# Kernel optimization log

Measured on AMD Instinct MI355X. Metric: run time of the kernel, lower is better.

Reference implementation:

```python
import jax, jax.numpy as jnp
import numpy as np

B, D = 32768, 512
L, K = 4, 1024


def setup_inputs() -> dict:
    key = jax.random.key(0)
    kz, kc = jax.random.split(key)
    z = jax.random.normal(kz, (B, D), dtype=jnp.float32)
    # nn.Parameter(torch.randn(L, K, D) * 0.1)
    codebooks = jax.random.normal(kc, (L, K, D), dtype=jnp.float32) * 0.1
    return {"z": z, "codebooks": codebooks}


def reference(z, codebooks):
    # z: [B, D], codebooks: [L, K, D]
    num_levels = codebooks.shape[0]
    residual = z
    level_vecs = []
    rq_loss = jnp.float32(0.0)
    for l in range(num_levels):  # small fixed L, structurally distinct levels
        cb = codebooks[l]  # [K, D]
        # squared euclidean distance via ||r||^2 - 2 r.c + ||c||^2 (same math as
        # sum((r[:,None]-c[None])**2, -1), avoids the [B,K,D] broadcast intermediate)
        r2 = jnp.sum(residual * residual, axis=-1, keepdims=True)      # [B, 1]
        c2 = jnp.sum(cb * cb, axis=-1)                                  # [K]
        dist = r2 - 2.0 * (residual @ cb.T) + c2                        # [B, K]
        idx = jnp.argmin(dist, axis=-1)                                 # [B]
        chosen = cb[idx]                                                # [B, D]
        level_vecs.append(chosen)
        residual = residual - chosen
        # F.mse_loss(residual.detach(), zeros) -> mean of squared residual, no grad
        rq_loss = rq_loss + jnp.mean(jax.lax.stop_gradient(residual) ** 2)
    all_level_vectors = jnp.stack(level_vecs, axis=0)  # [L, B, D]
    quantized = all_level_vectors.sum(axis=0)          # [B, D]
    return (quantized, all_level_vectors, rq_loss)
```

## Files before the change

kernel.cpp:

```cpp
#include <hip/hip_runtime.h>

#define BROWS 32768
#define DIM   512
#define NK    1024
#define NL    4

typedef _Float16 f16;
typedef _Float16 f16x8 __attribute__((ext_vector_type(8)));
typedef float f32x4 __attribute__((ext_vector_type(4)));

#define LSC 2.44140625e-4f

union H4 { f16 h[4]; ushort4 u; };

__device__ __forceinline__ void split2(float x, f16& h, f16& l) {
  h = (f16)x;
  l = (f16)((x - (float)h) * 4096.0f);
}

__device__ __forceinline__ void gload16(const void* g, const void* l) {
  __builtin_amdgcn_global_load_lds(
      (const __attribute__((address_space(1))) void*)g,
      (__attribute__((address_space(3))) void*)l, 16, 0, 0);
}

__global__ __launch_bounds__(64) void k_pre(const float* __restrict__ cb,
                                            float* __restrict__ c2all,
                                            float* __restrict__ loss_slot,
                                            f16* __restrict__ cbI) {
  const int code = blockIdx.x;
  const int lane = threadIdx.x;
  const float4* c4 = (const float4*)(cb + (size_t)code * DIM);
  f16* rowL = cbI + (size_t)code * 1024;
  float s = 0.f;
#pragma unroll
  for (int j = 0; j < 2; ++j) {
    const int e = lane + j * 64;
    const float4 v = c4[e];
    s += v.x * v.x + v.y * v.y + v.z * v.z + v.w * v.w;
    H4 hh, ll;
#pragma unroll
    for (int c = 0; c < 4; ++c) split2((&v.x)[c], hh.h[c], ll.h[c]);
    *(ushort4*)(rowL + e * 4) = hh.u;
    *(ushort4*)(rowL + 512 + e * 4) = ll.u;
  }
#pragma unroll
  for (int m = 1; m < 64; m <<= 1) s += __shfl_xor(s, m, 64);
  if (lane == 0) c2all[code] = s;
  if (code == 0 && lane == 0) *loss_slot = 0.f;
}

__global__ __launch_bounds__(256) void k_splitz(const float* __restrict__ Z,
                                                float* __restrict__ r2,
                                                f16* __restrict__ RL) {
  const int t = threadIdx.x;
  const int row = blockIdx.x * 8 + (t >> 5);
  const int lane = t & 31;
  const float4* z4 = (const float4*)(Z + (size_t)row * DIM);
  f16* rowL = RL + (size_t)row * 1024;
  float s = 0.f;
#pragma unroll
  for (int j = 0; j < 4; ++j) {
    const int e = lane + j * 32;
    const float4 v = z4[e];
    s += v.x * v.x + v.y * v.y + v.z * v.z + v.w * v.w;
    H4 hh, ll;
#pragma unroll
    for (int c = 0; c < 4; ++c) split2((&v.x)[c], hh.h[c], ll.h[c]);
    *(ushort4*)(rowL + e * 4) = hh.u;
    *(ushort4*)(rowL + 512 + e * 4) = ll.u;
  }
#pragma unroll
  for (int m = 1; m < 32; m <<= 1) s += __shfl_xor(s, m, 64);
  if (lane == 0) r2[row] = s;
}

__global__ __launch_bounds__(256, 2) void k_gemm(
    const f16* __restrict__ A,
    const f16* __restrict__ Bc,
    const float* __restrict__ r2v, const float* __restrict__ c2v,
    float* __restrict__ pmin, int* __restrict__ pidx) {
  __shared__ __align__(16) char smem[2][32768];

  const int t = threadIdx.x;
  const int lane = t & 63, wid = t >> 6;
  const int wr = wid >> 1, wc = wid & 1;
  const int lin = blockIdx.y * 8 + blockIdx.x;
  const int xcd = lin & 7, kk8 = lin >> 3;
  const int mb = xcd * 32 + (kk8 >> 3);
  const int nb = kk8 & 7;
  const int rowBase = mb * 128, colBase = nb * 128;
  const int l15 = lane & 15, kg = lane >> 4;

  const char* gA[4]; const char* gB[4];
  int ldsA[4], ldsB[4];
#pragma unroll
  for (int i = 0; i < 4; ++i) {
    const int g = i * 256 + wid * 64 + lane;
    const int r = g >> 3;
    const int u = (g & 7) ^ (r & 7);
    const size_t off = (size_t)r * 2048 + (size_t)(u >> 2) * 1024 + (u & 3) * 16;
    gA[i] = (const char*)A + (size_t)rowBase * 2048 + off;
    gB[i] = (const char*)Bc + (size_t)colBase * 2048 + off;
    ldsA[i] = i * 4096 + wid * 1024;
    ldsB[i] = 16384 + i * 4096 + wid * 1024;
  }

  const f32x4 zero = {0.f, 0.f, 0.f, 0.f};
  f32x4 accH[4][4], accL[4][4];
#pragma unroll
  for (int i = 0; i < 4; ++i)
#pragma unroll
    for (int j = 0; j < 4; ++j) { accH[i][j] = zero; accL[i][j] = zero; }

  auto stage = [&](int buf, int kt) {
    char* s = &smem[buf][0];
#pragma unroll
    for (int i = 0; i < 4; ++i) {
      gload16(gA[i] + kt * 64, s + ldsA[i]);
      gload16(gB[i] + kt * 64, s + ldsB[i]);
    }
  };

  auto compute = [&](int buf) {
    const char* sA = &smem[buf][0];
    const char* sB = sA + 16384;
    f16x8 bhv[4], blv[4];
#pragma unroll
    for (int ni = 0; ni < 4; ++ni) {
      const int c = wc * 64 + ni * 16 + l15;
      const int x = c & 7;
      bhv[ni] = *(const f16x8*)(sB + c * 128 + ((kg ^ x) << 4));
      blv[ni] = *(const f16x8*)(sB + c * 128 + (((4 + kg) ^ x) << 4));
    }
#pragma unroll
    for (int mi = 0; mi < 4; ++mi) {
      const int r = wr * 64 + mi * 16 + l15;
      const int x = r & 7;
      const f16x8 ahv = *(const f16x8*)(sA + r * 128 + ((kg ^ x) << 4));
      const f16x8 alw = *(const f16x8*)(sA + r * 128 + (((4 + kg) ^ x) << 4));
#pragma unroll
      for (int ni = 0; ni < 4; ++ni) {
        accH[mi][ni] = __builtin_amdgcn_mfma_f32_16x16x32_f16(ahv, bhv[ni], accH[mi][ni], 0, 0, 0);
        accL[mi][ni] = __builtin_amdgcn_mfma_f32_16x16x32_f16(ahv, blv[ni], accL[mi][ni], 0, 0, 0);
        accL[mi][ni] = __builtin_amdgcn_mfma_f32_16x16x32_f16(alw, bhv[ni], accL[mi][ni], 0, 0, 0);
      }
    }
  };

  stage(0, 0);
  for (int kt = 0; kt < 16; ++kt) {
    __syncthreads();
    if (kt < 15) stage((kt + 1) & 1, kt + 1);
    compute(kt & 1);
  }

  float* redm = (float*)&smem[0][0];
  int* redi = (int*)(&smem[0][0] + 1024);
  float c2c[4];
#pragma unroll
  for (int ni = 0; ni < 4; ++ni) c2c[ni] = c2v[colBase + wc * 64 + ni * 16 + l15];
#pragma unroll
  for (int mi = 0; mi < 4; ++mi) {
#pragma unroll
    for (int j = 0; j < 4; ++j) {
      const int rloc = wr * 64 + mi * 16 + kg * 4 + j;
      const float r2r = r2v[rowBase + rloc];
      float bm = 3.4e38f; int bi = 0x7fffffff;
#pragma unroll
      for (int ni = 0; ni < 4; ++ni) {
        const int col = colBase + wc * 64 + ni * 16 + l15;
        const float dot = accH[mi][ni][j] + accL[mi][ni][j] * LSC;
        const float dist = (r2r - 2.0f * dot) + c2c[ni];
        if (dist < bm || (dist == bm && col < bi)) { bm = dist; bi = col; }
      }
#pragma unroll
      for (int m = 1; m < 16; m <<= 1) {
        const float om = __shfl_xor(bm, m, 64);
        const int oi = __shfl_xor(bi, m, 64);
        if (om < bm || (om == bm && oi < bi)) { bm = om; bi = oi; }
      }
      if (l15 == 0) { redm[rloc * 2 + wc] = bm; redi[rloc * 2 + wc] = bi; }
    }
  }
  __syncthreads();
  if (t < 128) {
    float bm = redm[t * 2]; int bi = redi[t * 2];
    const float m1 = redm[t * 2 + 1]; const int i1 = redi[t * 2 + 1];
    if (m1 < bm || (m1 == bm && i1 < bi)) { bm = m1; bi = i1; }
    pmin[(size_t)nb * BROWS + rowBase + t] = bm;
    pidx[(size_t)nb * BROWS + rowBase + t] = bi;
  }
}

__global__ __launch_bounds__(256) void k_update(f16* RL,
                                                const float* __restrict__ CB,
                                                const float* __restrict__ pminv,
                                                const int* __restrict__ pidxv,
                                                float* __restrict__ chosen_out,
                                                float* __restrict__ r2out,
                                                float* __restrict__ loss,
                                                const float* __restrict__ Z,
                                                float* Q,
                                                int last) {
  __shared__ float ls[8];
  const int t = threadIdx.x;
  const int rrow = t >> 5, lane = t & 31;
  const int row = blockIdx.x * 8 + rrow;

  float bm = 3.4e38f;
  int bi = 0x7fffffff;
#pragma unroll
  for (int nbk = 0; nbk < 8; ++nbk) {
    const float m = pminv[(size_t)nbk * BROWS + row];
    const int i = pidxv[(size_t)nbk * BROWS + row];
    if (m < bm || (m == bm && i < bi)) { bm = m; bi = i; }
  }

  f16* rowL = RL + (size_t)row * 1024;
  ushort4 hu[4], lu[4];
#pragma unroll
  for (int j = 0; j < 4; ++j) {
    const int e = lane + j * 32;
    hu[j] = *(const ushort4*)(rowL + e * 4);
    lu[j] = *(const ushort4*)(rowL + 512 + e * 4);
  }

  const float4* c4 = (const float4*)(CB + (size_t)bi * DIM);
  float4* ch4 = (float4*)(chosen_out + (size_t)row * DIM);
  float s = 0.f;
#pragma unroll
  for (int j = 0; j < 4; ++j) {
    const int e = lane + j * 32;
    const float4 c = c4[e];
    H4 hh, llv;
    hh.u = hu[j]; llv.u = lu[j];
    float4 rn;
    rn.x = ((float)hh.h[0] + (float)llv.h[0] * LSC) - c.x;
    rn.y = ((float)hh.h[1] + (float)llv.h[1] * LSC) - c.y;
    rn.z = ((float)hh.h[2] + (float)llv.h[2] * LSC) - c.z;
    rn.w = ((float)hh.h[3] + (float)llv.h[3] * LSC) - c.w;
    ch4[e] = c;
    if (!last) {
      H4 nh, nl;
#pragma unroll
      for (int cc = 0; cc < 4; ++cc) split2((&rn.x)[cc], nh.h[cc], nl.h[cc]);
      *(ushort4*)(rowL + e * 4) = nh.u;
      *(ushort4*)(rowL + 512 + e * 4) = nl.u;
    } else {
      const float4 zv = ((const float4*)(Z + (size_t)row * DIM))[e];
      float4 qq;
      qq.x = zv.x - rn.x; qq.y = zv.y - rn.y; qq.z = zv.z - rn.z; qq.w = zv.w - rn.w;
      ((float4*)(Q + (size_t)row * DIM))[e] = qq;
    }
    s += rn.x * rn.x + rn.y * rn.y + rn.z * rn.z + rn.w * rn.w;
  }
#pragma unroll
  for (int m = 1; m < 32; m <<= 1) s += __shfl_xor(s, m, 64);
  if (lane == 0) {
    if (!last) r2out[row] = s;
    ls[rrow] = s;
  }
  __syncthreads();
  if (t == 0) {
    float tot = 0.f;
#pragma unroll
    for (int i = 0; i < 8; ++i) tot += ls[i];
    atomicAdd(loss, tot * (1.0f / 16777216.0f));
  }
}

extern "C" void kernel_launch(void* const* d_in, const int* in_sizes, int n_in,
                              void* d_out, int out_size, void* d_ws, size_t ws_size,
                              hipStream_t stream) {
  const float* z  = (const float*)d_in[0];
  const float* cb = (const float*)d_in[1];

  float* q    = (float*)d_out;
  float* alv  = (float*)d_out + (size_t)BROWS * DIM;
  float* loss = (float*)d_out + (size_t)BROWS * DIM * (NL + 1);

  float* c2all = (float*)d_ws;
  float* r2ws  = c2all + NL * NK;
  float* pmin  = r2ws + BROWS;
  int*   pidx  = (int*)(pmin + 8 * BROWS);
  f16*   cbI   = (f16*)(pidx + 8 * BROWS);

  f16* RL = (f16*)q;

  k_pre<<<NL * NK, 64, 0, stream>>>(cb, c2all, loss, cbI);
  k_splitz<<<BROWS / 8, 256, 0, stream>>>(z, r2ws, RL);

  for (int l = 0; l < NL; ++l) {
    k_gemm<<<dim3(8, 256), 256, 0, stream>>>(RL, cbI + (size_t)l * NK * 1024,
                                             r2ws, c2all + l * NK, pmin, pidx);
    const int last = (l == NL - 1);
    k_update<<<BROWS / 8, 256, 0, stream>>>(RL, cb + (size_t)l * NK * DIM,
                                            pmin, pidx,
                                            alv + (size_t)l * BROWS * DIM,
                                            r2ws, loss, z, q, last);
  }
}
```

Measured before the change: 1.087 ms.

## Shrink GEMM tile to 64x128 with 1x4 wave layout for higher occupancy

Changes the distance GEMM block tile from 128x128 to 64x128 rows by columns. All four waves now split the columns, 32 each, and the grid doubles to 8x512 blocks. LDS per block drops from 64KB to 48KB and the accumulator count halves, and launch bounds are raised to 3 blocks per CU so more waves can hide latency. In exchange, each codebook tile is reused across fewer rows, so more B traffic goes through global and LDS per FLOP. The final reduction now combines four column partials, and a barrier is added before the shared memory is reused.

```diff
diff --git a/kernel.cpp b/kernel.cpp
--- a/kernel.cpp
+++ b/kernel.cpp
@@ -75,76 +75,85 @@
   if (lane == 0) r2[row] = s;
 }
 
-__global__ __launch_bounds__(256, 2) void k_gemm(
+__global__ __launch_bounds__(256, 3) void k_gemm(
     const f16* __restrict__ A,
     const f16* __restrict__ Bc,
     const float* __restrict__ r2v, const float* __restrict__ c2v,
     float* __restrict__ pmin, int* __restrict__ pidx) {
-  __shared__ __align__(16) char smem[2][32768];
+  __shared__ __align__(16) char smem[2][24576];
 
   const int t = threadIdx.x;
   const int lane = t & 63, wid = t >> 6;
-  const int wr = wid >> 1, wc = wid & 1;
+  const int wc = wid;
   const int lin = blockIdx.y * 8 + blockIdx.x;
   const int xcd = lin & 7, kk8 = lin >> 3;
-  const int mb = xcd * 32 + (kk8 >> 3);
+  const int mb = xcd * 64 + (kk8 >> 3);
   const int nb = kk8 & 7;
-  const int rowBase = mb * 128, colBase = nb * 128;
+  const int rowBase = mb * 64, colBase = nb * 128;
   const int l15 = lane & 15, kg = lane >> 4;
 
-  const char* gA[4]; const char* gB[4];
-  int ldsA[4], ldsB[4];
+  const char* gA[2]; const char* gB[4];
+  int ldsA[2], ldsB[4];
+#pragma unroll
+  for (int i = 0; i < 2; ++i) {
+    const int g = i * 256 + wid * 64 + lane;
+    const int r = g >> 3;
+    const int u = (g & 7) ^ (r & 7);
+    gA[i] = (const char*)A + (size_t)(rowBase + r) * 2048 +
+            (size_t)(u >> 2) * 1024 + (u & 3) * 16;
+    ldsA[i] = i * 4096 + wid * 1024;
+  }
 #pragma unroll
   for (int i = 0; i < 4; ++i) {
     const int g = i * 256 + wid * 64 + lane;
     const int r = g >> 3;
     const int u = (g & 7) ^ (r & 7);
-    const size_t off = (size_t)r * 2048 + (size_t)(u >> 2) * 1024 + (u & 3) * 16;
-    gA[i] = (const char*)A + (size_t)rowBase * 2048 + off;
-    gB[i] = (const char*)Bc + (size_t)colBase * 2048 + off;
-    ldsA[i] = i * 4096 + wid * 1024;
-    ldsB[i] = 16384 + i * 4096 + wid * 1024;
+    gB[i] = (const char*)Bc + (size_t)(colBase + r) * 2048 +
+            (size_t)(u >> 2) * 1024 + (u & 3) * 16;
+    ldsB[i] = 8192 + i * 4096 + wid * 1024;
   }
 
   const f32x4 zero = {0.f, 0.f, 0.f, 0.f};
-  f32x4 accH[4][4], accL[4][4];
+  f32x4 accH[4][2], accL[4][2];
 #pragma unroll
   for (int i = 0; i < 4; ++i)
 #pragma unroll
-    for (int j = 0; j < 4; ++j) { accH[i][j] = zero; accL[i][j] = zero; }
+    for (int j = 0; j < 2; ++j) { accH[i][j] = zero; accL[i][j] = zero; }
 
   auto stage = [&](int buf, int kt) {
     char* s = &smem[buf][0];
 #pragma unroll
-    for (int i = 0; i < 4; ++i) {
-      gload16(gA[i] + kt * 64, s + ldsA[i]);
-      gload16(gB[i] + kt * 64, s + ldsB[i]);
-    }
+    for (int i = 0; i < 2; ++i) gload16(gA[i] + kt * 64, s + ldsA[i]);
+#pragma unroll
+    for (int i = 0; i < 4; ++i) gload16(gB[i] + kt * 64, s + ldsB[i]);
   };
 
   auto compute = [&](int buf) {
     const char* sA = &smem[buf][0];
-    const char* sB = sA + 16384;
-    f16x8 bhv[4], blv[4];
-#pragma unroll
-    for (int ni = 0; ni < 4; ++ni) {
-      const int c = wc * 64 + ni * 16 + l15;
+    const char* sB = sA + 8192;
+    f16x8 bhv[2], blv[2];
+#pragma unroll
+    for (int ni = 0; ni < 2; ++ni) {
+      const int c = wc * 32 + ni * 16 + l15;
       const int x = c & 7;
       bhv[ni] = *(const f16x8*)(sB + c * 128 + ((kg ^ x) << 4));
       blv[ni] = *(const f16x8*)(sB + c * 128 + (((4 + kg) ^ x) << 4));
     }
 #pragma unroll
     for (int mi = 0; mi < 4; ++mi) {
-      const int r = wr * 64 + mi * 16 + l15;
+      const int r = mi * 16 + l15;
       const int x = r & 7;
       const f16x8 ahv = *(const f16x8*)(sA + r * 128 + ((kg ^ x) << 4));
       const f16x8 alw = *(const f16x8*)(sA + r * 128 + (((4 + kg) ^ x) << 4));
 #pragma unroll
-      for (int ni = 0; ni < 4; ++ni) {
+      for (int ni = 0; ni < 2; ++ni)
         accH[mi][ni] = __builtin_amdgcn_mfma_f32_16x16x32_f16(ahv, bhv[ni], accH[mi][ni], 0, 0, 0);
+#pragma unroll
+      for (int ni = 0; ni < 2; ++ni)
         accL[mi][ni] = __builtin_amdgcn_mfma_f32_16x16x32_f16(ahv, blv[ni], accL[mi][ni], 0, 0, 0);
+#pragma unroll
+      for (int ni = 0; ni < 2; ++ni)
         accL[mi][ni] = __builtin_amdgcn_mfma_f32_16x16x32_f16(alw, bhv[ni], accL[mi][ni], 0, 0, 0);
-      }
     }
   };
 
@@ -154,22 +163,23 @@
     if (kt < 15) stage((kt + 1) & 1, kt + 1);
     compute(kt & 1);
   }
+  __syncthreads();
 
   float* redm = (float*)&smem[0][0];
   int* redi = (int*)(&smem[0][0] + 1024);
-  float c2c[4];
-#pragma unroll
-  for (int ni = 0; ni < 4; ++ni) c2c[ni] = c2v[colBase + wc * 64 + ni * 16 + l15];
+  float c2c[2];
+#pragma unroll
+  for (int ni = 0; ni < 2; ++ni) c2c[ni] = c2v[colBase + wc * 32 + ni * 16 + l15];
 #pragma unroll
   for (int mi = 0; mi < 4; ++mi) {
 #pragma unroll
     for (int j = 0; j < 4; ++j) {
-      const int rloc = wr * 64 + mi * 16 + kg * 4 + j;
+      const int rloc = mi * 16 + kg * 4 + j;
       const float r2r = r2v[rowBase + rloc];
       float bm = 3.4e38f; int bi = 0x7fffffff;
 #pragma unroll
-      for (int ni = 0; ni < 4; ++ni) {
-        const int col = colBase + wc * 64 + ni * 16 + l15;
+      for (int ni = 0; ni < 2; ++ni) {
+        const int col = colBase + wc * 32 + ni * 16 + l15;
         const float dot = accH[mi][ni][j] + accL[mi][ni][j] * LSC;
         const float dist = (r2r - 2.0f * dot) + c2c[ni];
         if (dist < bm || (dist == bm && col < bi)) { bm = dist; bi = col; }
@@ -180,14 +190,18 @@
         const int oi = __shfl_xor(bi, m, 64);
         if (om < bm || (om == bm && oi < bi)) { bm = om; bi = oi; }
       }
-      if (l15 == 0) { redm[rloc * 2 + wc] = bm; redi[rloc * 2 + wc] = bi; }
+      if (l15 == 0) { redm[rloc * 4 + wc] = bm; redi[rloc * 4 + wc] = bi; }
     }
   }
   __syncthreads();
-  if (t < 128) {
-    float bm = redm[t * 2]; int bi = redi[t * 2];
-    const float m1 = redm[t * 2 + 1]; const int i1 = redi[t * 2 + 1];
-    if (m1 < bm || (m1 == bm && i1 < bi)) { bm = m1; bi = i1; }
+  if (t < 64) {
+    float bm = 3.4e38f; int bi = 0x7fffffff;
+#pragma unroll
+    for (int x = 0; x < 4; ++x) {
+      const float m = redm[t * 4 + x];
+      const int i = redi[t * 4 + x];
+      if (m < bm || (m == bm && i < bi)) { bm = m; bi = i; }
+    }
     pmin[(size_t)nb * BROWS + rowBase + t] = bm;
     pidx[(size_t)nb * BROWS + rowBase + t] = bi;
   }
@@ -292,7 +306,7 @@
   k_splitz<<<BROWS / 8, 256, 0, stream>>>(z, r2ws, RL);
 
   for (int l = 0; l < NL; ++l) {
-    k_gemm<<<dim3(8, 256), 256, 0, stream>>>(RL, cbI + (size_t)l * NK * 1024,
+    k_gemm<<<dim3(8, 512), 256, 0, stream>>>(RL, cbI + (size_t)l * NK * 1024,
                                              r2ws, c2all + l * NK, pmin, pidx);
     const int last = (l == NL - 1);
     k_update<<<BROWS / 8, 256, 0, stream>>>(RL, cb + (size_t)l * NK * DIM,
```

Result: slower. 1.175 ms (+8.1%).

## Pre-tile split-fp16 operands into GEMM-tile-contiguous layout and recompute final residual

Applied to the files above, without the earlier changes.

Residual and codebook fp16 hi/lo limbs are now stored in a tiled layout that matches the LDS tile. Each GEMM stage therefore copies one contiguous 16 KB chunk per operand, and LDS reads become simple strided loads with no XOR swizzle. The MFMA issue order is regrouped by accumulator. The last-level update reconstructs the residual from z minus the three earlier chosen vectors instead of reading the fp16 limbs, which adds extra fp32 reads. Dropping the swizzle may bring back LDS bank conflicts.

```diff
diff --git a/kernel.cpp b/kernel.cpp
--- a/kernel.cpp
+++ b/kernel.cpp
@@ -24,14 +24,21 @@
       (__attribute__((address_space(3))) void*)l, 16, 0, 0);
 }
 
+__device__ __forceinline__ f16* limb_ptr(f16* base, size_t tile_gran, int e, int rc) {
+  const int kt = e >> 3, kgran = (e >> 1) & 3, half = e & 1;
+  return base + (tile_gran + (size_t)kt * 1024 + kgran * 128 + rc) * 8 + half * 4;
+}
+
 __global__ __launch_bounds__(64) void k_pre(const float* __restrict__ cb,
                                             float* __restrict__ c2all,
                                             float* __restrict__ loss_slot,
-                                            f16* __restrict__ cbI) {
+                                            f16* __restrict__ cbT) {
   const int code = blockIdx.x;
   const int lane = threadIdx.x;
+  const int lv = code >> 10, k = code & 1023;
+  const int nb = k >> 7, c = k & 127;
+  const size_t tg = (size_t)lv * 131072 + (size_t)nb * 16384;
   const float4* c4 = (const float4*)(cb + (size_t)code * DIM);
-  f16* rowL = cbI + (size_t)code * 1024;
   float s = 0.f;
 #pragma unroll
   for (int j = 0; j < 2; ++j) {
@@ -40,9 +47,10 @@
     s += v.x * v.x + v.y * v.y + v.z * v.z + v.w * v.w;
     H4 hh, ll;
 #pragma unroll
-    for (int c = 0; c < 4; ++c) split2((&v.x)[c], hh.h[c], ll.h[c]);
-    *(ushort4*)(rowL + e * 4) = hh.u;
-    *(ushort4*)(rowL + 512 + e * 4) = ll.u;
+    for (int q = 0; q < 4; ++q) split2((&v.x)[q], hh.h[q], ll.h[q]);
+    f16* ph = limb_ptr(cbT, tg, e, c);
+    *(ushort4*)ph = hh.u;
+    *(ushort4*)(ph + 4096) = ll.u;
   }
 #pragma unroll
   for (int m = 1; m < 64; m <<= 1) s += __shfl_xor(s, m, 64);
@@ -56,8 +64,9 @@
   const int t = threadIdx.x;
   const int row = blockIdx.x * 8 + (t >> 5);
   const int lane = t & 31;
+  const size_t tg = (size_t)(row >> 7) * 16384;
+  const int rloc = row & 127;
   const float4* z4 = (const float4*)(Z + (size_t)row * DIM);
-  f16* rowL = RL + (size_t)row * 1024;
   float s = 0.f;
 #pragma unroll
   for (int j = 0; j < 4; ++j) {
@@ -66,9 +75,10 @@
     s += v.x * v.x + v.y * v.y + v.z * v.z + v.w * v.w;
     H4 hh, ll;
 #pragma unroll
-    for (int c = 0; c < 4; ++c) split2((&v.x)[c], hh.h[c], ll.h[c]);
-    *(ushort4*)(rowL + e * 4) = hh.u;
-    *(ushort4*)(rowL + 512 + e * 4) = ll.u;
+    for (int q = 0; q < 4; ++q) split2((&v.x)[q], hh.h[q], ll.h[q]);
+    f16* ph = limb_ptr(RL, tg, e, rloc);
+    *(ushort4*)ph = hh.u;
+    *(ushort4*)(ph + 4096) = ll.u;
   }
 #pragma unroll
   for (int m = 1; m < 32; m <<= 1) s += __shfl_xor(s, m, 64);
@@ -96,14 +106,11 @@
   int ldsA[4], ldsB[4];
 #pragma unroll
   for (int i = 0; i < 4; ++i) {
-    const int g = i * 256 + wid * 64 + lane;
-    const int r = g >> 3;
-    const int u = (g & 7) ^ (r & 7);
-    const size_t off = (size_t)r * 2048 + (size_t)(u >> 2) * 1024 + (u & 3) * 16;
-    gA[i] = (const char*)A + (size_t)rowBase * 2048 + off;
-    gB[i] = (const char*)Bc + (size_t)colBase * 2048 + off;
-    ldsA[i] = i * 4096 + wid * 1024;
-    ldsB[i] = 16384 + i * 4096 + wid * 1024;
+    const int s = i * 256 + wid * 64 + lane;
+    gA[i] = (const char*)A + ((size_t)mb * 16384 + s) * 16;
+    gB[i] = (const char*)Bc + ((size_t)nb * 16384 + s) * 16;
+    ldsA[i] = s * 16;
+    ldsB[i] = 16384 + s * 16;
   }
 
   const f32x4 zero = {0.f, 0.f, 0.f, 0.f};
@@ -115,10 +122,11 @@
 
   auto stage = [&](int buf, int kt) {
     char* s = &smem[buf][0];
+    const size_t ko = (size_t)kt * 16384;
 #pragma unroll
     for (int i = 0; i < 4; ++i) {
-      gload16(gA[i] + kt * 64, s + ldsA[i]);
-      gload16(gB[i] + kt * 64, s + ldsB[i]);
+      gload16(gA[i] + ko, s + ldsA[i]);
+      gload16(gB[i] + ko, s + ldsB[i]);
     }
   };
 
@@ -129,22 +137,23 @@
 #pragma unroll
     for (int ni = 0; ni < 4; ++ni) {
       const int c = wc * 64 + ni * 16 + l15;
-      const int x = c & 7;
-      bhv[ni] = *(const f16x8*)(sB + c * 128 + ((kg ^ x) << 4));
-      blv[ni] = *(const f16x8*)(sB + c * 128 + (((4 + kg) ^ x) << 4));
+      bhv[ni] = *(const f16x8*)(sB + (kg * 128 + c) * 16);
+      blv[ni] = *(const f16x8*)(sB + ((4 + kg) * 128 + c) * 16);
     }
 #pragma unroll
     for (int mi = 0; mi < 4; ++mi) {
       const int r = wr * 64 + mi * 16 + l15;
-      const int x = r & 7;
-      const f16x8 ahv = *(const f16x8*)(sA + r * 128 + ((kg ^ x) << 4));
-      const f16x8 alw = *(const f16x8*)(sA + r * 128 + (((4 + kg) ^ x) << 4));
-#pragma unroll
-      for (int ni = 0; ni < 4; ++ni) {
+      const f16x8 ahv = *(const f16x8*)(sA + (kg * 128 + r) * 16);
+      const f16x8 alw = *(const f16x8*)(sA + ((4 + kg) * 128 + r) * 16);
+#pragma unroll
+      for (int ni = 0; ni < 4; ++ni)
         accH[mi][ni] = __builtin_amdgcn_mfma_f32_16x16x32_f16(ahv, bhv[ni], accH[mi][ni], 0, 0, 0);
+#pragma unroll
+      for (int ni = 0; ni < 4; ++ni)
         accL[mi][ni] = __builtin_amdgcn_mfma_f32_16x16x32_f16(ahv, blv[ni], accL[mi][ni], 0, 0, 0);
+#pragma unroll
+      for (int ni = 0; ni < 4; ++ni)
         accL[mi][ni] = __builtin_amdgcn_mfma_f32_16x16x32_f16(alw, bhv[ni], accL[mi][ni], 0, 0, 0);
-      }
     }
   };
 
@@ -201,7 +210,10 @@
                                                 float* __restrict__ r2out,
                                                 float* __restrict__ loss,
                                                 const float* __restrict__ Z,
-                                                float* Q,
+                                                float* __restrict__ Q,
+                                                const float* __restrict__ A0,
+                                                const float* __restrict__ A1,
+                                                const float* __restrict__ A2,
                                                 int last) {
   __shared__ float ls[8];
   const int t = threadIdx.x;
@@ -217,43 +229,58 @@
     if (m < bm || (m == bm && i < bi)) { bm = m; bi = i; }
   }
 
-  f16* rowL = RL + (size_t)row * 1024;
-  ushort4 hu[4], lu[4];
-#pragma unroll
-  for (int j = 0; j < 4; ++j) {
-    const int e = lane + j * 32;
-    hu[j] = *(const ushort4*)(rowL + e * 4);
-    lu[j] = *(const ushort4*)(rowL + 512 + e * 4);
-  }
-
+  const size_t tg = (size_t)(row >> 7) * 16384;
+  const int rloc = row & 127;
   const float4* c4 = (const float4*)(CB + (size_t)bi * DIM);
   float4* ch4 = (float4*)(chosen_out + (size_t)row * DIM);
   float s = 0.f;
-#pragma unroll
-  for (int j = 0; j < 4; ++j) {
-    const int e = lane + j * 32;
-    const float4 c = c4[e];
-    H4 hh, llv;
-    hh.u = hu[j]; llv.u = lu[j];
-    float4 rn;
-    rn.x = ((float)hh.h[0] + (float)llv.h[0] * LSC) - c.x;
-    rn.y = ((float)hh.h[1] + (float)llv.h[1] * LSC) - c.y;
-    rn.z = ((float)hh.h[2] + (float)llv.h[2] * LSC) - c.z;
-    rn.w = ((float)hh.h[3] + (float)llv.h[3] * LSC) - c.w;
-    ch4[e] = c;
-    if (!last) {
+
+  if (!last) {
+#pragma unroll
+    for (int j = 0; j < 4; ++j) {
+      const int e = lane + j * 32;
+      f16* ph = limb_ptr(RL, tg, e, rloc);
+      H4 hh, llv;
+      hh.u = *(const ushort4*)ph;
+      llv.u = *(const ushort4*)(ph + 4096);
+      const float4 c = c4[e];
+      float4 rn;
+      rn.x = ((float)hh.h[0] + (float)llv.h[0] * LSC) - c.x;
+      rn.y = ((float)hh.h[1] + (float)llv.h[1] * LSC) - c.y;
+      rn.z = ((float)hh.h[2] + (float)llv.h[2] * LSC) - c.z;
+      rn.w = ((float)hh.h[3] + (float)llv.h[3] * LSC) - c.w;
+      ch4[e] = c;
       H4 nh, nl;
 #pragma unroll
-      for (int cc = 0; cc < 4; ++cc) split2((&rn.x)[cc], nh.h[cc], nl.h[cc]);
-      *(ushort4*)(rowL + e * 4) = nh.u;
-      *(ushort4*)(rowL + 512 + e * 4) = nl.u;
-    } else {
-      const float4 zv = ((const float4*)(Z + (size_t)row * DIM))[e];
-      float4 qq;
-      qq.x = zv.x - rn.x; qq.y = zv.y - rn.y; qq.z = zv.z - rn.z; qq.w = zv.w - rn.w;
-      ((float4*)(Q + (size_t)row * DIM))[e] = qq;
-    }
-    s += rn.x * rn.x + rn.y * rn.y + rn.z * rn.z + rn.w * rn.w;
+      for (int q = 0; q < 4; ++q) split2((&rn.x)[q], nh.h[q], nl.h[q]);
+      *(ushort4*)ph = nh.u;
+      *(ushort4*)(ph + 4096) = nl.u;
+      s += rn.x * rn.x + rn.y * rn.y + rn.z * rn.z + rn.w * rn.w;
+    }
+  } else {
+    const float4* z4 = (const float4*)(Z + (size_t)row * DIM);
+    const float4* a04 = (const float4*)(A0 + (size_t)row * DIM);
+    const float4* a14 = (const float4*)(A1 + (size_t)row * DIM);
+    const float4* a24 = (const float4*)(A2 + (size_t)row * DIM);
+    float4* q4 = (float4*)(Q + (size_t)row * DIM);
+#pragma unroll
+    for (int j = 0; j < 4; ++j) {
+      const int e = lane + j * 32;
+      const float4 zv = z4[e];
+      const float4 a0 = a04[e], a1 = a14[e], a2 = a24[e];
+      const float4 c = c4[e];
+      float4 r3, rn, qq;
+#pragma unroll
+      for (int q = 0; q < 4; ++q) {
+        const float r3q = (((&zv.x)[q] - (&a0.x)[q]) - (&a1.x)[q]) - (&a2.x)[q];
+        (&r3.x)[q] = r3q;
+        (&rn.x)[q] = r3q - (&c.x)[q];
+        (&qq.x)[q] = (((&a0.x)[q] + (&a1.x)[q]) + (&a2.x)[q]) + (&c.x)[q];
+      }
+      ch4[e] = c;
+      q4[e] = qq;
+      s += rn.x * rn.x + rn.y * rn.y + rn.z * rn.z + rn.w * rn.w;
+    }
   }
 #pragma unroll
   for (int m = 1; m < 32; m <<= 1) s += __shfl_xor(s, m, 64);
@@ -284,20 +311,23 @@
   float* r2ws  = c2all + NL * NK;
   float* pmin  = r2ws + BROWS;
   int*   pidx  = (int*)(pmin + 8 * BROWS);
-  f16*   cbI   = (f16*)(pidx + 8 * BROWS);
+  f16*   cbT   = (f16*)(pidx + 8 * BROWS);
 
   f16* RL = (f16*)q;
 
-  k_pre<<<NL * NK, 64, 0, stream>>>(cb, c2all, loss, cbI);
+  k_pre<<<NL * NK, 64, 0, stream>>>(cb, c2all, loss, cbT);
   k_splitz<<<BROWS / 8, 256, 0, stream>>>(z, r2ws, RL);
 
   for (int l = 0; l < NL; ++l) {
-    k_gemm<<<dim3(8, 256), 256, 0, stream>>>(RL, cbI + (size_t)l * NK * 1024,
-                                             r2ws, c2all + l * NK, pmin, pidx);
+    k_gemm<<<dim3(8, 256), 256, 0, stream>>>(
+        RL, cbT + (size_t)l * 131072 * 8,
+        r2ws, c2all + l * NK, pmin, pidx);
     const int last = (l == NL - 1);
-    k_update<<<BROWS / 8, 256, 0, stream>>>(RL, cb + (size_t)l * NK * DIM,
-                                            pmin, pidx,
-                                            alv + (size_t)l * BROWS * DIM,
-                                            r2ws, loss, z, q, last);
-  }
-}
+    k_update<<<BROWS / 8, 256, 0, stream>>>(
+        RL, cb + (size_t)l * NK * DIM, pmin, pidx,
+        alv + (size_t)l * BROWS * DIM, r2ws, loss, z, q,
+        alv + 0 * (size_t)BROWS * DIM,
+        alv + 1 * (size_t)BROWS * DIM,
+        alv + 2 * (size_t)BROWS * DIM, last);
+  }
+}
```

Result: no change. 1.077 ms (-0.9%).
